# Kernel tuning notes

Measured on AMD Instinct MI355X. Metric: run time of the kernel, lower is better.

The kernel has to match this reference:

```python
import jax, jax.numpy as jnp
import numpy as np

EMBED_DIM = 1024
NUM_HEADS = 16
HEAD_DIM = EMBED_DIM // NUM_HEADS


def setup_inputs() -> dict:
    key = jax.random.key(0)
    ks = jax.random.split(key, 5)
    B, S, D = 2, 2048, EMBED_DIM
    scale = 1.0 / np.sqrt(D)
    x = jax.random.normal(ks[0], (B, S, D), dtype=jnp.float32)
    W_qkv = jax.random.normal(ks[1], (D, 3 * D), dtype=jnp.float32) * scale
    b_qkv = jnp.zeros((3 * D,), dtype=jnp.float32)
    W_out = jax.random.normal(ks[2], (D, D), dtype=jnp.float32) * scale
    b_out = jnp.zeros((D,), dtype=jnp.float32)
    return {"x": x, "W_qkv": W_qkv, "b_qkv": b_qkv, "W_out": W_out, "b_out": b_out}


def reference(x, W_qkv, b_qkv, W_out, b_out):
    B, S, D = x.shape
    H, Hd = NUM_HEADS, HEAD_DIM
    qkv = x @ W_qkv + b_qkv                       # [B,S,3D]
    qkv = qkv.reshape(B, S, 3, H, Hd)
    q = qkv[:, :, 0].transpose(0, 2, 1, 3)        # [B,H,S,Hd]
    k = qkv[:, :, 1].transpose(0, 2, 1, 3)
    v = qkv[:, :, 2].transpose(0, 2, 1, 3)
    scores = jnp.einsum('bhqd,bhkd->bhqk', q, k) / np.sqrt(Hd)  # [B,H,S,S]
    causal = jnp.tril(jnp.ones((S, S), dtype=bool))
    scores = jnp.where(causal[None, None], scores, -jnp.inf)
    attn = jax.nn.softmax(scores, axis=-1)
    out = jnp.einsum('bhqk,bhkd->bhqd', attn, v)  # [B,H,S,Hd]
    out = out.transpose(0, 2, 1, 3).reshape(B, S, D)
    return out @ W_out + b_out
```

## Files before the change

### kernel.cpp

```cpp
#include <hip/hip_runtime.h>
#include <hip/hip_bf16.h>
#include <math.h>

#define EMBED_DIM 1024
#define NUM_HEADS 16
#define HEAD_DIM 64
#define BATCH 2
#define SEQ 2048

using short8  = __attribute__((ext_vector_type(8))) short;
using floatx4 = __attribute__((ext_vector_type(4))) float;

__device__ __forceinline__ ushort f2bf(float f) {
    unsigned u = __float_as_uint(f);
    u = (u + 0x7FFFu + ((u >> 16) & 1u)) >> 16;
    return (ushort)u;
}

__device__ __forceinline__ void load_lds16(const ushort* g, ushort* l) {
    __builtin_amdgcn_global_load_lds(
        (const __attribute__((address_space(1))) void*)g,
        (__attribute__((address_space(3))) void*)l, 16, 0, 0);
}

__device__ __forceinline__ void tc_tile(
    const float* __restrict__ W, ushort* __restrict__ Wt,
    int K, int N, int n0, int k0, float (*t)[65])
{
    const int c = threadIdx.x & 63, r0 = (threadIdx.x >> 6) * 16;
    #pragma unroll
    for (int r = 0; r < 16; ++r)
        t[r0 + r][c] = W[(size_t)(k0 + r0 + r) * N + n0 + c];
    __syncthreads();
    #pragma unroll
    for (int r = 0; r < 16; ++r)
        Wt[(size_t)(n0 + r0 + r) * K + k0 + c] = f2bf(t[c][r0 + r]);
}

__global__ __launch_bounds__(256) void prep_all(
    const float* __restrict__ x, const float* __restrict__ W_qkv,
    const float* __restrict__ W_out,
    ushort* __restrict__ xb, ushort* __restrict__ Wqb_t, ushort* __restrict__ Wob_t)
{
    __shared__ float t[64][65];
    const int bx = blockIdx.x;
    if (bx < 4096) {
        int i = (bx * 256 + threadIdx.x) * 4;
        float4 v = *(const float4*)&x[i];
        ushort4 o = { f2bf(v.x), f2bf(v.y), f2bf(v.z), f2bf(v.w) };
        *(ushort4*)&xb[i] = o;
    } else if (bx < 4096 + 768) {
        int b = bx - 4096;
        tc_tile(W_qkv, Wqb_t, 1024, 3072, (b % 48) * 64, (b / 48) * 64, t);
    } else {
        int b = bx - 4864;
        tc_tile(W_out, Wob_t, 1024, 1024, (b % 16) * 64, (b / 16) * 64, t);
    }
}

#define GK 1024

__device__ __forceinline__ void gemm_core(
    const ushort* __restrict__ A, const ushort* __restrict__ Bt,
    int m0, int n0, ushort* As, ushort* Bs, floatx4 acc[4][4])
{
    const int tid  = threadIdx.x;
    const int w    = tid >> 6;
    const int lane = tid & 63;
    const int col  = lane & 15;
    const int quad = lane >> 4;
    const int wm   = w >> 1, wn = w & 1;

    #pragma unroll
    for (int i = 0; i < 4; ++i)
        #pragma unroll
        for (int j = 0; j < 4; ++j)
            acc[i][j] = (floatx4){0.f, 0.f, 0.f, 0.f};

    const int o0   = w * 2048 + lane * 16;
    const int row0 = o0 >> 6;
    const int ke0  = (o0 & 63) >> 1;

    for (int k0 = 0; k0 < GK; k0 += 32) {
        #pragma unroll
        for (int t = 0; t < 2; ++t) {
            const int row = row0 + t * 16;
            ushort* la = As + ((w * 2048 + t * 1024) >> 1);
            ushort* lb = Bs + ((w * 2048 + t * 1024) >> 1);
            load_lds16(A  + (size_t)(m0 + row) * GK + k0 + ke0, la);
            load_lds16(Bt + (size_t)(n0 + row) * GK + k0 + ke0, lb);
        }
        __syncthreads();

        short8 af[4], bf[4];
        #pragma unroll
        for (int i = 0; i < 4; ++i)
            af[i] = *(const short8*)&As[(wm * 64 + i * 16 + col) * 32 + quad * 8];
        #pragma unroll
        for (int j = 0; j < 4; ++j)
            bf[j] = *(const short8*)&Bs[(wn * 64 + j * 16 + col) * 32 + quad * 8];
        #pragma unroll
        for (int i = 0; i < 4; ++i)
            #pragma unroll
            for (int j = 0; j < 4; ++j)
                acc[i][j] = __builtin_amdgcn_mfma_f32_16x16x32_bf16(af[i], bf[j], acc[i][j], 0, 0, 0);

        __syncthreads();
    }
}

__global__ __launch_bounds__(256) void gemm_qkv_mfma(
    const ushort* __restrict__ A, const ushort* __restrict__ Bt,
    const float* __restrict__ bias,
    ushort* __restrict__ Qb, ushort* __restrict__ Kb, ushort* __restrict__ Vt)
{
    __shared__ __align__(16) ushort As[128 * 32];
    __shared__ __align__(16) ushort Bs[128 * 32];
    const int n0 = blockIdx.x * 128;
    const int m0 = blockIdx.y * 128;

    floatx4 acc[4][4];
    gemm_core(A, Bt, m0, n0, As, Bs, acc);

    const int lane = threadIdx.x & 63;
    const int w    = threadIdx.x >> 6;
    const int col  = lane & 15, quad = lane >> 4;
    const int wm   = w >> 1, wn = w & 1;

    #pragma unroll
    for (int j = 0; j < 4; ++j) {
        const int n = n0 + wn * 64 + j * 16 + col;
        const float bj = bias[n];
        const int part = n >> 10;
        const int h = (n >> 6) & 15;
        const int d = n & 63;
        #pragma unroll
        for (int i = 0; i < 4; ++i)
            #pragma unroll
            for (int r = 0; r < 4; ++r) {
                const int m = m0 + wm * 64 + i * 16 + quad * 4 + r;
                const int b = m >> 11, s = m & 2047;
                const int bh = b * 16 + h;
                const ushort bv = f2bf(acc[i][j][r] + bj);
                if (part == 0)      Qb[((size_t)bh * SEQ + s) * 64 + d] = bv;
                else if (part == 1) Kb[((size_t)bh * SEQ + s) * 64 + d] = bv;
                else                Vt[((size_t)bh * 64 + d) * SEQ + s] = bv;
            }
    }
}

__global__ __launch_bounds__(256) void gemm_out_mfma(
    const ushort* __restrict__ A, const ushort* __restrict__ Bt,
    const float* __restrict__ bias, float* __restrict__ out)
{
    __shared__ __align__(16) ushort As[128 * 32];
    __shared__ __align__(16) ushort Bs[128 * 32];
    const int n0 = blockIdx.x * 128;
    const int m0 = blockIdx.y * 128;

    floatx4 acc[4][4];
    gemm_core(A, Bt, m0, n0, As, Bs, acc);

    const int lane = threadIdx.x & 63;
    const int w    = threadIdx.x >> 6;
    const int col  = lane & 15, quad = lane >> 4;
    const int wm   = w >> 1, wn = w & 1;

    #pragma unroll
    for (int j = 0; j < 4; ++j) {
        const int n = n0 + wn * 64 + j * 16 + col;
        const float bj = bias[n];
        #pragma unroll
        for (int i = 0; i < 4; ++i)
            #pragma unroll
            for (int r = 0; r < 4; ++r) {
                const int m = m0 + wm * 64 + i * 16 + quad * 4 + r;
                out[(size_t)m * EMBED_DIM + n] = acc[i][j][r] + bj;
            }
    }
}

#define LP 72
#define EXP2_SCALE 0.18033688011112042f

__global__ __launch_bounds__(256) void attn_fused(
    const ushort* __restrict__ Qb, const ushort* __restrict__ Kb,
    const ushort* __restrict__ Vt, ushort* __restrict__ out)
{
    const int id = blockIdx.x;
    const int qt = 31 - (id >> 5);
    const int bh = id & 31;
    const int b  = bh >> 4, h = bh & 15;
    const int q0 = qt * 64;

    __shared__ ushort Qs[64 * LP];
    __shared__ ushort Ks[64 * LP];
    __shared__ ushort Vs[64 * LP];
    __shared__ ushort Ps[64 * LP];

    const int tid  = threadIdx.x;
    const int w    = tid >> 6;
    const int lane = tid & 63;
    const int col  = lane & 15;
    const int quad = lane >> 4;

    const ushort* Qg = Qb + ((size_t)bh * SEQ + q0) * 64;
    for (int i = tid; i < 64 * 8; i += 256) {
        int r = i >> 3, c8 = (i & 7) * 8;
        *(short8*)&Qs[r * LP + c8] = *(const short8*)&Qg[r * 64 + c8];
    }

    floatx4 acc_o[4];
    #pragma unroll
    for (int dbi = 0; dbi < 4; ++dbi) acc_o[dbi] = (floatx4){0.f, 0.f, 0.f, 0.f};
    float l_r[4] = {0.f, 0.f, 0.f, 0.f};

    for (int kt = 0; kt <= qt; ++kt) {
        const int k0 = kt * 64;
        __syncthreads();
        const ushort* Kg = Kb + ((size_t)bh * SEQ + k0) * 64;
        const ushort* Vg = Vt + (size_t)bh * 64 * SEQ + k0;
        for (int i = tid; i < 64 * 8; i += 256) {
            int r = i >> 3, c8 = (i & 7) * 8;
            *(short8*)&Ks[r * LP + c8] = *(const short8*)&Kg[r * 64 + c8];
            *(short8*)&Vs[r * LP + c8] = *(const short8*)&Vg[(size_t)r * SEQ + c8];
        }
        __syncthreads();

        short8 a0 = *(const short8*)&Qs[(w * 16 + col) * LP + quad * 8];
        short8 a1 = *(const short8*)&Qs[(w * 16 + col) * LP + 32 + quad * 8];
        floatx4 s_acc[4];
        #pragma unroll
        for (int kb = 0; kb < 4; ++kb) {
            s_acc[kb] = (floatx4){0.f, 0.f, 0.f, 0.f};
            short8 b0 = *(const short8*)&Ks[(kb * 16 + col) * LP + quad * 8];
            short8 b1 = *(const short8*)&Ks[(kb * 16 + col) * LP + 32 + quad * 8];
            s_acc[kb] = __builtin_amdgcn_mfma_f32_16x16x32_bf16(a0, b0, s_acc[kb], 0, 0, 0);
            s_acc[kb] = __builtin_amdgcn_mfma_f32_16x16x32_bf16(a1, b1, s_acc[kb], 0, 0, 0);
        }

        const bool diag = (kt == qt);
        #pragma unroll
        for (int kb = 0; kb < 4; ++kb)
            #pragma unroll
            for (int r = 0; r < 4; ++r) {
                float s = s_acc[kb][r];
                if (diag && (kb * 16 + col > w * 16 + quad * 4 + r)) s = -INFINITY;
                float p = exp2f(s * EXP2_SCALE);
                l_r[r] += p;
                Ps[(w * 16 + quad * 4 + r) * LP + kb * 16 + col] =
                    (ushort)((__float_as_uint(p) + 0x8000u) >> 16);
            }

        short8 pa0 = *(const short8*)&Ps[(w * 16 + col) * LP + quad * 8];
        short8 pa1 = *(const short8*)&Ps[(w * 16 + col) * LP + 32 + quad * 8];
        #pragma unroll
        for (int dbi = 0; dbi < 4; ++dbi) {
            short8 vb0 = *(const short8*)&Vs[(dbi * 16 + col) * LP + quad * 8];
            short8 vb1 = *(const short8*)&Vs[(dbi * 16 + col) * LP + 32 + quad * 8];
            acc_o[dbi] = __builtin_amdgcn_mfma_f32_16x16x32_bf16(pa0, vb0, acc_o[dbi], 0, 0, 0);
            acc_o[dbi] = __builtin_amdgcn_mfma_f32_16x16x32_bf16(pa1, vb1, acc_o[dbi], 0, 0, 0);
        }
    }

    float inv_l[4];
    #pragma unroll
    for (int r = 0; r < 4; ++r) {
        float lr = l_r[r];
        lr += __shfl_xor(lr, 1);
        lr += __shfl_xor(lr, 2);
        lr += __shfl_xor(lr, 4);
        lr += __shfl_xor(lr, 8);
        inv_l[r] = 1.f / lr;
    }

    #pragma unroll
    for (int dbi = 0; dbi < 4; ++dbi)
        #pragma unroll
        for (int r = 0; r < 4; ++r) {
            int q = q0 + w * 16 + quad * 4 + r;
            int d = dbi * 16 + col;
            out[((size_t)(b * SEQ + q)) * EMBED_DIM + h * 64 + d] = f2bf(acc_o[dbi][r] * inv_l[r]);
        }
}

extern "C" void kernel_launch(void* const* d_in, const int* in_sizes, int n_in,
                              void* d_out, int out_size, void* d_ws, size_t ws_size,
                              hipStream_t stream)
{
    const float* x     = (const float*)d_in[0];
    const float* W_qkv = (const float*)d_in[1];
    const float* b_qkv = (const float*)d_in[2];
    const float* W_out = (const float*)d_in[3];
    const float* b_out = (const float*)d_in[4];
    float* out = (float*)d_out;

    const int M  = BATCH * SEQ;
    const int D  = EMBED_DIM;
    const int N1 = 3 * D;
    const size_t HE = (size_t)BATCH * NUM_HEADS * SEQ * 64;

    ushort* xb    = (ushort*)d_ws;
    ushort* Wqb_t = xb + (size_t)M * D;
    ushort* Wob_t = Wqb_t + (size_t)D * N1;
    ushort* Qb    = Wob_t + (size_t)D * D;
    ushort* Kb    = Qb + HE;
    ushort* Vt    = Kb + HE;
    ushort* attnb = Vt + HE;

    prep_all<<<5120, 256, 0, stream>>>(x, W_qkv, W_out, xb, Wqb_t, Wob_t);

    gemm_qkv_mfma<<<dim3(N1 / 128, M / 128), 256, 0, stream>>>(
        xb, Wqb_t, b_qkv, Qb, Kb, Vt);

    attn_fused<<<dim3(32 * 32), 256, 0, stream>>>(Qb, Kb, Vt, attnb);

    gemm_out_mfma<<<dim3(D / 128, M / 128), 256, 0, stream>>>(
        attnb, Wob_t, b_out, out);
}
```

Measured before the change: 205.3 us.

## Load attention Q/K/V tiles directly to LDS in MFMA fragment order

Q, K and V tiles are now copied with global_load_lds in a layout where each lane's MFMA operand is a contiguous 16-byte chunk, replacing register-staged padded-row copies. Q fragments are hoisted into registers once, outside the key loop. The diagonal mask is split into its own branch so non-diagonal tiles skip the per-element compare. This is meant to cut VGPR traffic, LDS bank conflicts and address math in the inner loop. Loads are still issued synchronously between barriers, with no double buffering.

```diff
diff --git a/kernel.cpp b/kernel.cpp
--- a/kernel.cpp
+++ b/kernel.cpp
@@ -193,9 +193,9 @@
     const int b  = bh >> 4, h = bh & 15;
     const int q0 = qt * 64;
 
-    __shared__ ushort Qs[64 * LP];
-    __shared__ ushort Ks[64 * LP];
-    __shared__ ushort Vs[64 * LP];
+    __shared__ __align__(16) ushort Qs[8 * 512];
+    __shared__ __align__(16) ushort Ks[8 * 512];
+    __shared__ __align__(16) ushort Vs[8 * 512];
     __shared__ ushort Ps[64 * LP];
 
     const int tid  = threadIdx.x;
@@ -204,60 +204,87 @@
     const int col  = lane & 15;
     const int quad = lane >> 4;
 
-    const ushort* Qg = Qb + ((size_t)bh * SEQ + q0) * 64;
-    for (int i = tid; i < 64 * 8; i += 256) {
-        int r = i >> 3, c8 = (i & 7) * 8;
-        *(short8*)&Qs[r * LP + c8] = *(const short8*)&Qg[r * 64 + c8];
-    }
+    {
+        const ushort* Qg = Qb + ((size_t)bh * SEQ + q0) * 64;
+        #pragma unroll
+        for (int t = 0; t < 2; ++t) {
+            const ushort* g = Qg + (size_t)(w * 16 + col) * 64 + t * 32 + quad * 8;
+            load_lds16(g, &Qs[(w * 2 + t) * 512]);
+        }
+    }
+
+    const ushort* kg[2];
+    const ushort* vg[2];
+    #pragma unroll
+    for (int t = 0; t < 2; ++t) {
+        const int c = w * 2 + t;
+        const int rb = c >> 1, hf = c & 1;
+        kg[t] = Kb + (size_t)bh * SEQ * 64 + (size_t)(rb * 16 + col) * 64 + hf * 32 + quad * 8;
+        vg[t] = Vt + (size_t)bh * 64 * SEQ + (size_t)(rb * 16 + col) * SEQ + hf * 32 + quad * 8;
+    }
+
+    __syncthreads();
+    const short8 a0 = *(const short8*)&Qs[(w * 2 + 0) * 512 + lane * 8];
+    const short8 a1 = *(const short8*)&Qs[(w * 2 + 1) * 512 + lane * 8];
 
     floatx4 acc_o[4];
     #pragma unroll
     for (int dbi = 0; dbi < 4; ++dbi) acc_o[dbi] = (floatx4){0.f, 0.f, 0.f, 0.f};
     float l_r[4] = {0.f, 0.f, 0.f, 0.f};
 
+    const int myrow = w * 16 + quad * 4;
+
     for (int kt = 0; kt <= qt; ++kt) {
-        const int k0 = kt * 64;
         __syncthreads();
-        const ushort* Kg = Kb + ((size_t)bh * SEQ + k0) * 64;
-        const ushort* Vg = Vt + (size_t)bh * 64 * SEQ + k0;
-        for (int i = tid; i < 64 * 8; i += 256) {
-            int r = i >> 3, c8 = (i & 7) * 8;
-            *(short8*)&Ks[r * LP + c8] = *(const short8*)&Kg[r * 64 + c8];
-            *(short8*)&Vs[r * LP + c8] = *(const short8*)&Vg[(size_t)r * SEQ + c8];
+        #pragma unroll
+        for (int t = 0; t < 2; ++t) {
+            load_lds16(kg[t], &Ks[(w * 2 + t) * 512]);
+            load_lds16(vg[t], &Vs[(w * 2 + t) * 512]);
+            kg[t] += 64 * 64;
+            vg[t] += 64;
         }
         __syncthreads();
 
-        short8 a0 = *(const short8*)&Qs[(w * 16 + col) * LP + quad * 8];
-        short8 a1 = *(const short8*)&Qs[(w * 16 + col) * LP + 32 + quad * 8];
         floatx4 s_acc[4];
         #pragma unroll
         for (int kb = 0; kb < 4; ++kb) {
-            s_acc[kb] = (floatx4){0.f, 0.f, 0.f, 0.f};
-            short8 b0 = *(const short8*)&Ks[(kb * 16 + col) * LP + quad * 8];
-            short8 b1 = *(const short8*)&Ks[(kb * 16 + col) * LP + 32 + quad * 8];
-            s_acc[kb] = __builtin_amdgcn_mfma_f32_16x16x32_bf16(a0, b0, s_acc[kb], 0, 0, 0);
-            s_acc[kb] = __builtin_amdgcn_mfma_f32_16x16x32_bf16(a1, b1, s_acc[kb], 0, 0, 0);
-        }
-
-        const bool diag = (kt == qt);
-        #pragma unroll
-        for (int kb = 0; kb < 4; ++kb)
-            #pragma unroll
-            for (int r = 0; r < 4; ++r) {
-                float s = s_acc[kb][r];
-                if (diag && (kb * 16 + col > w * 16 + quad * 4 + r)) s = -INFINITY;
-                float p = exp2f(s * EXP2_SCALE);
-                l_r[r] += p;
-                Ps[(w * 16 + quad * 4 + r) * LP + kb * 16 + col] =
-                    (ushort)((__float_as_uint(p) + 0x8000u) >> 16);
-            }
+            short8 b0 = *(const short8*)&Ks[(kb * 2 + 0) * 512 + lane * 8];
+            short8 b1 = *(const short8*)&Ks[(kb * 2 + 1) * 512 + lane * 8];
+            floatx4 z = (floatx4){0.f, 0.f, 0.f, 0.f};
+            z = __builtin_amdgcn_mfma_f32_16x16x32_bf16(a0, b0, z, 0, 0, 0);
+            z = __builtin_amdgcn_mfma_f32_16x16x32_bf16(a1, b1, z, 0, 0, 0);
+            s_acc[kb] = z;
+        }
+
+        if (kt == qt) {
+            #pragma unroll
+            for (int kb = 0; kb < 4; ++kb)
+                #pragma unroll
+                for (int r = 0; r < 4; ++r) {
+                    float p = (kb * 16 + col > myrow + r)
+                                ? 0.f : exp2f(s_acc[kb][r] * EXP2_SCALE);
+                    l_r[r] += p;
+                    Ps[(myrow + r) * LP + kb * 16 + col] =
+                        (ushort)((__float_as_uint(p) + 0x8000u) >> 16);
+                }
+        } else {
+            #pragma unroll
+            for (int kb = 0; kb < 4; ++kb)
+                #pragma unroll
+                for (int r = 0; r < 4; ++r) {
+                    float p = exp2f(s_acc[kb][r] * EXP2_SCALE);
+                    l_r[r] += p;
+                    Ps[(myrow + r) * LP + kb * 16 + col] =
+                        (ushort)((__float_as_uint(p) + 0x8000u) >> 16);
+                }
+        }
 
         short8 pa0 = *(const short8*)&Ps[(w * 16 + col) * LP + quad * 8];
         short8 pa1 = *(const short8*)&Ps[(w * 16 + col) * LP + 32 + quad * 8];
         #pragma unroll
         for (int dbi = 0; dbi < 4; ++dbi) {
-            short8 vb0 = *(const short8*)&Vs[(dbi * 16 + col) * LP + quad * 8];
-            short8 vb1 = *(const short8*)&Vs[(dbi * 16 + col) * LP + 32 + quad * 8];
+            short8 vb0 = *(const short8*)&Vs[(dbi * 2 + 0) * 512 + lane * 8];
+            short8 vb1 = *(const short8*)&Vs[(dbi * 2 + 1) * 512 + lane * 8];
             acc_o[dbi] = __builtin_amdgcn_mfma_f32_16x16x32_bf16(pa0, vb0, acc_o[dbi], 0, 0, 0);
             acc_o[dbi] = __builtin_amdgcn_mfma_f32_16x16x32_bf16(pa1, vb1, acc_o[dbi], 0, 0, 0);
         }
```

Measured after the change: 199.5 us. 2.8% less time.
